# Performance work log

Measured on AMD Instinct MI355X. Metric: run time of the kernel, lower is better.

Reference implementation:

```python
import jax, jax.numpy as jnp
import numpy as np

N_VISIBLE = 4096
N_HIDDEN = 4096
BATCH = 8192


def setup_inputs() -> dict:
    key = jax.random.key(0)
    k_x, k_w = jax.random.split(key)
    input_data = jax.random.uniform(k_x, (BATCH, N_VISIBLE), dtype=jnp.float32)
    # xavier_uniform with sigmoid gain (=1.0): limit = sqrt(6/(fan_in+fan_out))
    limit = float(np.sqrt(6.0 / (N_VISIBLE + N_HIDDEN)))
    W = jax.random.uniform(k_w, (N_VISIBLE, N_HIDDEN), dtype=jnp.float32,
                           minval=-limit, maxval=limit)
    hidden_bias = jnp.zeros((N_HIDDEN,), dtype=jnp.float32)
    return {"input_data": input_data, "W": W, "hidden_bias": hidden_bias}


def reference(input_data, W, hidden_bias):
    # RBM.sample_hidden_2 (forward): sigmoid(x @ W + b), batched over samples.
    # (The torch code loops per sample with host syncs; same math, vectorized.)
    hid_prob = jax.nn.sigmoid(jnp.matmul(input_data, W) + hidden_bias)
    return hid_prob
```

## Files before the change

kernel.cpp:

```cpp
#include <hip/hip_runtime.h>
#include <cstdint>

#define MDIM 8192
#define NDIM 4096
#define KDIM 4096
#define NT (KDIM / 64)

typedef __bf16 bf16x8 __attribute__((ext_vector_type(8)));
typedef float f32x4 __attribute__((ext_vector_type(4)));

#define MFMA16 __builtin_amdgcn_mfma_f32_16x16x32_bf16

__device__ __forceinline__ void gload_lds16(const void* g, void* l) {
    __builtin_amdgcn_global_load_lds(
        (const __attribute__((address_space(1))) uint32_t*)g,
        (__attribute__((address_space(3))) uint32_t*)l, 16, 0, 0);
}

__device__ __forceinline__ unsigned short bf16_bits(float f) {
    __bf16 b = (__bf16)f;
    return __builtin_bit_cast(unsigned short, b);
}

__device__ __forceinline__ int detect_f32(const void* X) {
    int ok = 1;
    if (threadIdx.x < 128) {
        unsigned short h = ((const unsigned short*)X)[threadIdx.x];
        ok = (h <= 0x3F80);
    }
    return __syncthreads_and(ok) ? 0 : 1;
}

__global__ __launch_bounds__(256) void prep(const void* __restrict__ X,
                                            const void* __restrict__ W,
                                            __bf16* __restrict__ Xb,
                                            __bf16* __restrict__ WT) {
    const int f32 = detect_f32(X);
    const int t = threadIdx.x;
    if (blockIdx.x < 8192) {
        if (!f32) return;
        const float* Xf = (const float*)X;
        const long base = ((long)blockIdx.x * 256 + t) * 16;
#pragma unroll
        for (int c = 0; c < 2; ++c) {
            float4 v0 = *(const float4*)(Xf + base + c * 8);
            float4 v1 = *(const float4*)(Xf + base + c * 8 + 4);
            unsigned short r[8] = {bf16_bits(v0.x), bf16_bits(v0.y),
                                   bf16_bits(v0.z), bf16_bits(v0.w),
                                   bf16_bits(v1.x), bf16_bits(v1.y),
                                   bf16_bits(v1.z), bf16_bits(v1.w)};
            *(uint4*)(Xb + base + c * 8) = *(const uint4*)r;
        }
        return;
    }
    __shared__ unsigned short tile[64 * 65];
    const int bid = blockIdx.x - 8192;
    const int n0 = (bid & 63) * 64;
    const int k0 = (bid >> 6) * 64;
    if (f32) {
        const float* Wf = (const float*)W;
#pragma unroll
        for (int p = 0; p < 4; ++p) {
            const int ch = p * 256 + t;
            const int kr = ch >> 4;
            const int nc = ch & 15;
            float4 v = *(const float4*)(Wf + (long)(k0 + kr) * NDIM + n0 + nc * 4);
            tile[(nc * 4 + 0) * 65 + kr] = bf16_bits(v.x);
            tile[(nc * 4 + 1) * 65 + kr] = bf16_bits(v.y);
            tile[(nc * 4 + 2) * 65 + kr] = bf16_bits(v.z);
            tile[(nc * 4 + 3) * 65 + kr] = bf16_bits(v.w);
        }
    } else {
        const __bf16* Wb = (const __bf16*)W;
#pragma unroll
        for (int p = 0; p < 2; ++p) {
            const int ch = p * 256 + t;
            const int kr = ch >> 3;
            const int nc = ch & 7;
            uint4 v = *(const uint4*)(Wb + (long)(k0 + kr) * NDIM + n0 + nc * 8);
            const unsigned short* e = (const unsigned short*)&v;
#pragma unroll
            for (int i = 0; i < 8; ++i) tile[(nc * 8 + i) * 65 + kr] = e[i];
        }
    }
    __syncthreads();
#pragma unroll
    for (int p = 0; p < 2; ++p) {
        const int ch = p * 256 + t;
        const int nr = ch >> 3;
        const int kc = ch & 7;
        unsigned short r[8];
#pragma unroll
        for (int i = 0; i < 8; ++i) r[i] = tile[nr * 65 + kc * 8 + i];
        *(uint4*)(WT + (long)(n0 + nr) * KDIM + k0 + kc * 8) = *(uint4*)r;
    }
}

__global__ __launch_bounds__(256) void transpose_w(const void* __restrict__ X,
                                                   const void* __restrict__ W,
                                                   __bf16* __restrict__ WT) {
    __shared__ unsigned short tile[64 * 65];
    const int f32 = detect_f32(X);
    const int t = threadIdx.x;
    const int k0 = blockIdx.y * 64;
    const int n0 = blockIdx.x * 64;
    if (f32) {
        const float* Wf = (const float*)W;
#pragma unroll
        for (int p = 0; p < 4; ++p) {
            const int ch = p * 256 + t;
            const int kr = ch >> 4;
            const int nc = ch & 15;
            float4 v = *(const float4*)(Wf + (long)(k0 + kr) * NDIM + n0 + nc * 4);
            tile[(nc * 4 + 0) * 65 + kr] = bf16_bits(v.x);
            tile[(nc * 4 + 1) * 65 + kr] = bf16_bits(v.y);
            tile[(nc * 4 + 2) * 65 + kr] = bf16_bits(v.z);
            tile[(nc * 4 + 3) * 65 + kr] = bf16_bits(v.w);
        }
    } else {
        const __bf16* Wb = (const __bf16*)W;
#pragma unroll
        for (int p = 0; p < 2; ++p) {
            const int ch = p * 256 + t;
            const int kr = ch >> 3;
            const int nc = ch & 7;
            uint4 v = *(const uint4*)(Wb + (long)(k0 + kr) * NDIM + n0 + nc * 8);
            const unsigned short* e = (const unsigned short*)&v;
#pragma unroll
            for (int i = 0; i < 8; ++i) tile[(nc * 8 + i) * 65 + kr] = e[i];
        }
    }
    __syncthreads();
#pragma unroll
    for (int p = 0; p < 2; ++p) {
        const int ch = p * 256 + t;
        const int nr = ch >> 3;
        const int kc = ch & 7;
        unsigned short r[8];
#pragma unroll
        for (int i = 0; i < 8; ++i) r[i] = tile[nr * 65 + kc * 8 + i];
        *(uint4*)(WT + (long)(n0 + nr) * KDIM + k0 + kc * 8) = *(uint4*)r;
    }
}

#define P_OPEN()                                        \
    do {                                                \
        __builtin_amdgcn_sched_barrier(0);              \
        __builtin_amdgcn_s_barrier();                   \
        asm volatile("s_waitcnt lgkmcnt(0)" ::: "memory"); \
        __builtin_amdgcn_sched_barrier(0);              \
    } while (0)
#define P_CLOSE()                          \
    do {                                   \
        __builtin_amdgcn_sched_barrier(0); \
        __builtin_amdgcn_s_barrier();      \
    } while (0)

__global__ __launch_bounds__(512, 2) void gemm256(
    const void* __restrict__ X, const __bf16* __restrict__ Xb,
    const __bf16* __restrict__ WT, const void* __restrict__ bias,
    void* __restrict__ out) {
    __shared__ __bf16 sA[2][256][64];
    __shared__ __bf16 sB[2][256][64];
    const int f32 = detect_f32(X);
    const __bf16* __restrict__ Abf = f32 ? Xb : (const __bf16*)X;
    const int t = threadIdx.x;
    const int lane = t & 63;
    const int wid = t >> 6;
    const int wm = wid >> 2;
    const int wn = wid & 3;
    const int lrow = lane & 15;
    const int quad = lane >> 4;
    const int l7 = lrow & 7;

    const int flat = blockIdx.x;
    const int swz = (flat & 7) * (512 / 8) + (flat >> 3);
    const long m0 = (long)(swz >> 4) * 256;
    const long n0 = (long)(swz & 15) * 256;

    const int r8 = lane >> 3;
    const int c8 = lane & 7;
    const int cs = (c8 ^ r8) * 8;
    const __bf16* gA = Abf + (m0 + wid * 8 + r8) * KDIM + cs;
    const __bf16* gB = WT + (n0 + wid * 8 + r8) * KDIM + cs;
    __bf16* lA = &sA[0][wid * 8][0];
    __bf16* lB = &sB[0][wid * 8][0];

    auto stage_a = [&](int tt2) {
        const long off = (long)(tt2 & 1) * 16384;
        const long ko = (long)(tt2 & (NT - 1)) * 64;
        gload_lds16(gA + ko, lA + off);
        gload_lds16(gA + (long)64 * KDIM + ko, lA + off + 4096);
        gload_lds16(gA + (long)128 * KDIM + ko, lA + off + 8192);
        gload_lds16(gA + (long)192 * KDIM + ko, lA + off + 12288);
    };
    auto stage_b = [&](int tt2, int h) {
        const long off = (long)(tt2 & 1) * 16384 + (long)h * 8192;
        const long ko = (long)(tt2 & (NT - 1)) * 64;
        gload_lds16(gB + (long)(h * 128) * KDIM + ko, lB + off);
        gload_lds16(gB + (long)(h * 128 + 64) * KDIM + ko, lB + off + 4096);
    };

    const int soff0 = (quad ^ l7) * 8;
    const int soff1 = ((4 + quad) ^ l7) * 8;
    const __bf16* pa = &sA[0][wm * 128 + lrow][0];
    const __bf16* pb = &sB[0][wn * 64 + lrow][0];

    f32x4 acc[8][4] = {};

    stage_a(0);
    stage_b(0, 0);
    stage_b(0, 1);
    stage_b(1, 0);
    stage_a(1);
    __builtin_amdgcn_sched_barrier(0);
    asm volatile("s_waitcnt vmcnt(6)" ::: "memory");
    __builtin_amdgcn_sched_barrier(0);
    __builtin_amdgcn_s_barrier();

#pragma unroll 1
    for (int tt = 0; tt < NT; ++tt) {
        const int db = tt & 1;
        const __bf16* paT = pa + db * 16384;
        const __bf16* pbT = pb + db * 16384;
        bf16x8 aF[4][2], bF[4][2];
#pragma unroll
        for (int j = 0; j < 4; ++j) {
            bF[j][0] = *(const bf16x8*)(pbT + j * 1024 + soff0);
            bF[j][1] = *(const bf16x8*)(pbT + j * 1024 + soff1);
        }
#pragma unroll
        for (int i = 0; i < 4; ++i) {
            aF[i][0] = *(const bf16x8*)(paT + i * 1024 + soff0);
            aF[i][1] = *(const bf16x8*)(paT + i * 1024 + soff1);
        }
        stage_b(tt + 1, 1);
        P_OPEN();
        __builtin_amdgcn_s_setprio(1);
#pragma unroll
        for (int i = 0; i < 4; ++i)
#pragma unroll
            for (int j = 0; j < 2; ++j) {
                acc[i][j] = MFMA16(aF[i][0], bF[j][0], acc[i][j], 0, 0, 0);
                acc[i][j] = MFMA16(aF[i][1], bF[j][1], acc[i][j], 0, 0, 0);
            }
        __builtin_amdgcn_s_setprio(0);
        P_CLOSE();
        stage_b(tt + 2, 0);
        P_OPEN();
        __builtin_amdgcn_s_setprio(1);
#pragma unroll
        for (int i = 0; i < 4; ++i)
#pragma unroll
            for (int j = 2; j < 4; ++j) {
                acc[i][j] = MFMA16(aF[i][0], bF[j][0], acc[i][j], 0, 0, 0);
                acc[i][j] = MFMA16(aF[i][1], bF[j][1], acc[i][j], 0, 0, 0);
            }
        __builtin_amdgcn_s_setprio(0);
        P_CLOSE();
#pragma unroll
        for (int i = 0; i < 4; ++i) {
            aF[i][0] = *(const bf16x8*)(paT + 4096 + i * 1024 + soff0);
            aF[i][1] = *(const bf16x8*)(paT + 4096 + i * 1024 + soff1);
        }
        P_OPEN();
        __builtin_amdgcn_s_setprio(1);
#pragma unroll
        for (int i = 0; i < 4; ++i)
#pragma unroll
            for (int j = 2; j < 4; ++j) {
                acc[i + 4][j] = MFMA16(aF[i][0], bF[j][0], acc[i + 4][j], 0, 0, 0);
                acc[i + 4][j] = MFMA16(aF[i][1], bF[j][1], acc[i + 4][j], 0, 0, 0);
            }
        __builtin_amdgcn_s_setprio(0);
        P_CLOSE();
        stage_a(tt + 2);
        P_OPEN();
        __builtin_amdgcn_s_setprio(1);
#pragma unroll
        for (int i = 0; i < 4; ++i)
#pragma unroll
            for (int j = 0; j < 2; ++j) {
                acc[i + 4][j] = MFMA16(aF[i][0], bF[j][0], acc[i + 4][j], 0, 0, 0);
                acc[i + 4][j] = MFMA16(aF[i][1], bF[j][1], acc[i + 4][j], 0, 0, 0);
            }
        __builtin_amdgcn_s_setprio(0);
        __builtin_amdgcn_sched_barrier(0);
        asm volatile("s_waitcnt vmcnt(6)" ::: "memory");
        __builtin_amdgcn_sched_barrier(0);
        __builtin_amdgcn_s_barrier();
    }

    const int crow0 = (int)m0 + wm * 128 + quad * 4;
    if (f32) {
        float* of = (float*)out;
        const float* bf = (const float*)bias;
#pragma unroll
        for (int j = 0; j < 4; ++j) {
            const int col = (int)n0 + wn * 64 + j * 16 + lrow;
            const float bv = bf[col];
#pragma unroll
            for (int i = 0; i < 8; ++i) {
                const long rbase = (long)(crow0 + i * 16) * NDIM + col;
#pragma unroll
                for (int r = 0; r < 4; ++r) {
                    const float x = acc[i][j][r] + bv;
                    of[rbase + (long)r * NDIM] = 1.0f / (1.0f + __expf(-x));
                }
            }
        }
    } else {
        __bf16* ob = (__bf16*)out;
        const __bf16* bb = (const __bf16*)bias;
#pragma unroll
        for (int j = 0; j < 4; ++j) {
            const int col = (int)n0 + wn * 64 + j * 16 + lrow;
            const float bv = (float)bb[col];
#pragma unroll
            for (int i = 0; i < 8; ++i) {
                const long rbase = (long)(crow0 + i * 16) * NDIM + col;
#pragma unroll
                for (int r = 0; r < 4; ++r) {
                    const float x = acc[i][j][r] + bv;
                    ob[rbase + (long)r * NDIM] = (__bf16)(1.0f / (1.0f + __expf(-x)));
                }
            }
        }
    }
}

template <int MODE>
__global__ __launch_bounds__(256) void gemm_bias_sigmoid(
    const void* __restrict__ X, const __bf16* __restrict__ Xb,
    const void* __restrict__ Wp, const __bf16* __restrict__ WT,
    const void* __restrict__ bias, void* __restrict__ out) {
    __shared__ __bf16 sA[128 * 64];
    __shared__ __bf16 sB[128 * 64];
    const int f32 = detect_f32(X);
    const int t = threadIdx.x;
    const int lane = t & 63;
    const int wid = t >> 6;
    const int m0 = blockIdx.y * 128;
    const int n0 = blockIdx.x * 128;
    const int wm = (wid & 1) * 64;
    const int wn = (wid >> 1) * 64;
    const int lrow = lane & 15;
    const int quad = lane >> 4;

    f32x4 acc[4][4] = {};

    {
        const int srow = t >> 2;
        const int schk = t & 3;
        __bf16* ldsA = sA + wid * 512;
        __bf16* ldsB = sB + wid * 512;
        const int arow = t >> 1;
        const int acol = (t & 1) * 16;
        const int fp = t & 15;
        const int fc = t >> 4;
        uint32_t* sB32 = (uint32_t*)sB;

        auto compute = [&]() {
            bf16x8 aF[4], bFr[4];
            const __bf16* pa = sA + (wm + lrow) * 32 + quad * 8;
            const __bf16* pb = sB + (wn + lrow) * 32 + quad * 8;
#pragma unroll
            for (int i = 0; i < 4; ++i) aF[i] = *(const bf16x8*)(pa + i * 512);
#pragma unroll
            for (int j = 0; j < 4; ++j) bFr[j] = *(const bf16x8*)(pb + j * 512);
#pragma unroll
            for (int i = 0; i < 4; ++i)
#pragma unroll
                for (int j = 0; j < 4; ++j)
                    acc[i][j] = MFMA16(aF[i], bFr[j], acc[i][j], 0, 0, 0);
        };

        if (MODE == 1 && !f32) {
            const __bf16* gA = (const __bf16*)X + (long)(m0 + srow) * KDIM + schk * 8;
            const __bf16* gB = WT + (long)(n0 + srow) * KDIM + schk * 8;
            for (int kt = 0; kt < KDIM / 32; ++kt) {
                const __bf16* a0 = gA + kt * 32;
                gload_lds16(a0, ldsA);
                gload_lds16(a0 + (long)64 * KDIM, ldsA + 2048);
                const __bf16* b0 = gB + kt * 32;
                gload_lds16(b0, ldsB);
                gload_lds16(b0 + (long)64 * KDIM, ldsB + 2048);
                __syncthreads();
                compute();
                __syncthreads();
            }
        } else if (MODE == 1) {
            const float* Xf = (const float*)X;
            const __bf16* gB = WT + (long)(n0 + srow) * KDIM + schk * 8;
            for (int kt = 0; kt < KDIM / 32; ++kt) {
                const __bf16* b0 = gB + kt * 32;
                gload_lds16(b0, ldsB);
                gload_lds16(b0 + (long)64 * KDIM, ldsB + 2048);
                const float* ap = Xf + (long)(m0 + arow) * KDIM + kt * 32 + acol;
                float4 v0 = *(const float4*)(ap);
                float4 v1 = *(const float4*)(ap + 4);
                float4 v2 = *(const float4*)(ap + 8);
                float4 v3 = *(const float4*)(ap + 12);
                unsigned short r[16] = {
                    bf16_bits(v0.x), bf16_bits(v0.y), bf16_bits(v0.z), bf16_bits(v0.w),
                    bf16_bits(v1.x), bf16_bits(v1.y), bf16_bits(v1.z), bf16_bits(v1.w),
                    bf16_bits(v2.x), bf16_bits(v2.y), bf16_bits(v2.z), bf16_bits(v2.w),
                    bf16_bits(v3.x), bf16_bits(v3.y), bf16_bits(v3.z), bf16_bits(v3.w)};
                *(uint4*)(sA + arow * 32 + acol) = *(const uint4*)(r);
                *(uint4*)(sA + arow * 32 + acol + 8) = *(const uint4*)(r + 8);
                __syncthreads();
                compute();
                __syncthreads();
            }
        } else if (MODE == 2 && !f32) {
            const __bf16* gA = (const __bf16*)X + (long)(m0 + srow) * KDIM + schk * 8;
            const __bf16* Wb = (const __bf16*)Wp;
            for (int kt = 0; kt < KDIM / 32; ++kt) {
                const __bf16* a0 = gA + kt * 32;
                gload_lds16(a0, ldsA);
                gload_lds16(a0 + (long)64 * KDIM, ldsA + 2048);
                const __bf16* w0 = Wb + (long)(kt * 32 + 2 * fp) * NDIM + n0 + fc * 8;
                uint4 g0 = *(const uint4*)(w0);
                uint4 g1 = *(const uint4*)(w0 + NDIM);
                const unsigned short* e0 = (const unsigned short*)&g0;
                const unsigned short* e1 = (const unsigned short*)&g1;
#pragma unroll
                for (int i = 0; i < 8; ++i)
                    sB32[(fc * 8 + i) * 16 + fp] =
                        (uint32_t)e0[i] | ((uint32_t)e1[i] << 16);
                __syncthreads();
                compute();
                __syncthreads();
            }
        } else if (MODE == 2) {
            const float* Xf = (const float*)X;
            const float* Wf = (const float*)Wp;
            for (int kt = 0; kt < KDIM / 32; ++kt) {
                const float* ap = Xf + (long)(m0 + arow) * KDIM + kt * 32 + acol;
                float4 v0 = *(const float4*)(ap);
                float4 v1 = *(const float4*)(ap + 4);
                float4 v2 = *(const float4*)(ap + 8);
                float4 v3 = *(const float4*)(ap + 12);
                unsigned short r[16] = {
                    bf16_bits(v0.x), bf16_bits(v0.y), bf16_bits(v0.z), bf16_bits(v0.w),
                    bf16_bits(v1.x), bf16_bits(v1.y), bf16_bits(v1.z), bf16_bits(v1.w),
                    bf16_bits(v2.x), bf16_bits(v2.y), bf16_bits(v2.z), bf16_bits(v2.w),
                    bf16_bits(v3.x), bf16_bits(v3.y), bf16_bits(v3.z), bf16_bits(v3.w)};
                *(uint4*)(sA + arow * 32 + acol) = *(const uint4*)(r);
                *(uint4*)(sA + arow * 32 + acol + 8) = *(const uint4*)(r + 8);
                const float* w0 = Wf + (long)(kt * 32 + 2 * fp) * NDIM + n0 + fc * 8;
                float4 u0 = *(const float4*)(w0);
                float4 u1 = *(const float4*)(w0 + 4);
                float4 u2 = *(const float4*)(w0 + NDIM);
                float4 u3 = *(const float4*)(w0 + NDIM + 4);
                float k0v[8] = {u0.x, u0.y, u0.z, u0.w, u1.x, u1.y, u1.z, u1.w};
                float k1v[8] = {u2.x, u2.y, u2.z, u2.w, u3.x, u3.y, u3.z, u3.w};
#pragma unroll
                for (int i = 0; i < 8; ++i)
                    sB32[(fc * 8 + i) * 16 + fp] =
                        (uint32_t)bf16_bits(k0v[i]) |
                        ((uint32_t)bf16_bits(k1v[i]) << 16);
                __syncthreads();
                compute();
                __syncthreads();
            }
        }
    }

    const int crow = m0 + wm + quad * 4;
    if (f32) {
        float* of = (float*)out;
        const float* bf = (const float*)bias;
#pragma unroll
        for (int j = 0; j < 4; ++j) {
            const int col = n0 + wn + j * 16 + lrow;
            const float bv = bf[col];
#pragma unroll
            for (int i = 0; i < 4; ++i) {
                const long rbase = (long)(crow + i * 16) * NDIM + col;
#pragma unroll
                for (int r = 0; r < 4; ++r) {
                    const float x = acc[i][j][r] + bv;
                    of[rbase + (long)r * NDIM] = 1.0f / (1.0f + __expf(-x));
                }
            }
        }
    } else {
        __bf16* ob = (__bf16*)out;
        const __bf16* bb = (const __bf16*)bias;
#pragma unroll
        for (int j = 0; j < 4; ++j) {
            const int col = n0 + wn + j * 16 + lrow;
            const float bv = (float)bb[col];
#pragma unroll
            for (int i = 0; i < 4; ++i) {
                const long rbase = (long)(crow + i * 16) * NDIM + col;
#pragma unroll
                for (int r = 0; r < 4; ++r) {
                    const float x = acc[i][j][r] + bv;
                    ob[rbase + (long)r * NDIM] = (__bf16)(1.0f / (1.0f + __expf(-x)));
                }
            }
        }
    }
}

extern "C" void kernel_launch(void* const* d_in, const int* in_sizes, int n_in,
                              void* d_out, int out_size, void* d_ws,
                              size_t ws_size, hipStream_t stream) {
    const void* X = d_in[0];
    const void* W = d_in[1];
    const void* bias = d_in[2];

    const size_t wt_bytes = (size_t)KDIM * NDIM * sizeof(__bf16);
    const size_t xb_bytes = (size_t)MDIM * KDIM * sizeof(__bf16);

    if (ws_size >= wt_bytes + xb_bytes) {
        __bf16* WT = (__bf16*)d_ws;
        __bf16* Xb = (__bf16*)((char*)d_ws + wt_bytes);
        prep<<<8192 + 4096, 256, 0, stream>>>(X, W, Xb, WT);
        gemm256<<<dim3((MDIM / 256) * (NDIM / 256)), 512, 0, stream>>>(
            X, Xb, WT, bias, d_out);
    } else if (ws_size >= wt_bytes) {
        __bf16* WT = (__bf16*)d_ws;
        transpose_w<<<dim3(NDIM / 64, KDIM / 64), 256, 0, stream>>>(X, W, WT);
        dim3 gg(NDIM / 128, MDIM / 128);
        gemm_bias_sigmoid<1><<<gg, 256, 0, stream>>>(X, nullptr, W, WT, bias, d_out);
    } else {
        dim3 gg(NDIM / 128, MDIM / 128);
        gemm_bias_sigmoid<2><<<gg, 256, 0, stream>>>(X, nullptr, W, nullptr, bias, d_out);
    }
}
```

Measured before the change: 559.3 us.

## Restructure GEMM main loop into templated double-buffer k-tiles with staggered fragment loads

```diff
diff --git a/kernel.cpp b/kernel.cpp
--- a/kernel.cpp
+++ b/kernel.cpp
@@ -40,16 +40,14 @@
     if (blockIdx.x < 8192) {
         if (!f32) return;
         const float* Xf = (const float*)X;
-        const long base = ((long)blockIdx.x * 256 + t) * 16;
-#pragma unroll
-        for (int c = 0; c < 2; ++c) {
-            float4 v0 = *(const float4*)(Xf + base + c * 8);
-            float4 v1 = *(const float4*)(Xf + base + c * 8 + 4);
-            unsigned short r[8] = {bf16_bits(v0.x), bf16_bits(v0.y),
-                                   bf16_bits(v0.z), bf16_bits(v0.w),
-                                   bf16_bits(v1.x), bf16_bits(v1.y),
-                                   bf16_bits(v1.z), bf16_bits(v1.w)};
-            *(uint4*)(Xb + base + c * 8) = *(const uint4*)r;
+        const long xbase = (long)blockIdx.x * 4096;
+#pragma unroll
+        for (int rr = 0; rr < 4; ++rr) {
+            const long idx = xbase + rr * 1024 + t * 4;
+            float4 v = *(const float4*)(Xf + idx);
+            unsigned short r[4] = {bf16_bits(v.x), bf16_bits(v.y),
+                                   bf16_bits(v.z), bf16_bits(v.w)};
+            *(uint2*)(Xb + idx) = *(const uint2*)r;
         }
         return;
     }
@@ -143,18 +141,105 @@
     }
 }
 
-#define P_OPEN()                                        \
-    do {                                                \
-        __builtin_amdgcn_sched_barrier(0);              \
-        __builtin_amdgcn_s_barrier();                   \
+#define P_OPEN()                                           \
+    do {                                                   \
+        __builtin_amdgcn_sched_barrier(0);                 \
+        __builtin_amdgcn_s_barrier();                      \
         asm volatile("s_waitcnt lgkmcnt(0)" ::: "memory"); \
-        __builtin_amdgcn_sched_barrier(0);              \
+        __builtin_amdgcn_sched_barrier(0);                 \
     } while (0)
 #define P_CLOSE()                          \
     do {                                   \
         __builtin_amdgcn_sched_barrier(0); \
         __builtin_amdgcn_s_barrier();      \
     } while (0)
+
+template <int DBOFF>
+__device__ __forceinline__ void ktile(const __bf16* pa, const __bf16* pb,
+                                      const __bf16* gA, const __bf16* gB,
+                                      __bf16* lA, __bf16* lB, long ko2,
+                                      int soff0, int soff1,
+                                      f32x4 (&acc)[8][4]) {
+    const __bf16* paT = pa + DBOFF;
+    const __bf16* pbT = pb + DBOFF;
+    bf16x8 aF[4][2], bF[4][2];
+#pragma unroll
+    for (int j = 0; j < 2; ++j) {
+        bF[j][0] = *(const bf16x8*)(pbT + j * 1024 + soff0);
+        bF[j][1] = *(const bf16x8*)(pbT + j * 1024 + soff1);
+    }
+#pragma unroll
+    for (int i = 0; i < 4; ++i) {
+        aF[i][0] = *(const bf16x8*)(paT + i * 1024 + soff0);
+        aF[i][1] = *(const bf16x8*)(paT + i * 1024 + soff1);
+    }
+    asm volatile("s_waitcnt lgkmcnt(8)" ::: "memory");
+    P_OPEN();
+    __builtin_amdgcn_s_setprio(1);
+#pragma unroll
+    for (int kk = 0; kk < 2; ++kk)
+#pragma unroll
+        for (int i = 0; i < 4; ++i)
+#pragma unroll
+            for (int j = 0; j < 2; ++j)
+                acc[i][j] = MFMA16(aF[i][kk], bF[j][kk], acc[i][j], 0, 0, 0);
+    __builtin_amdgcn_s_setprio(0);
+    P_CLOSE();
+#pragma unroll
+    for (int j = 2; j < 4; ++j) {
+        bF[j][0] = *(const bf16x8*)(pbT + j * 1024 + soff0);
+        bF[j][1] = *(const bf16x8*)(pbT + j * 1024 + soff1);
+    }
+    P_OPEN();
+    __builtin_amdgcn_s_setprio(1);
+#pragma unroll
+    for (int kk = 0; kk < 2; ++kk)
+#pragma unroll
+        for (int i = 0; i < 4; ++i)
+#pragma unroll
+            for (int j = 2; j < 4; ++j)
+                acc[i][j] = MFMA16(aF[i][kk], bF[j][kk], acc[i][j], 0, 0, 0);
+    __builtin_amdgcn_s_setprio(0);
+    P_CLOSE();
+#pragma unroll
+    for (int i = 0; i < 4; ++i) {
+        aF[i][0] = *(const bf16x8*)(paT + (4 + i) * 1024 + soff0);
+        aF[i][1] = *(const bf16x8*)(paT + (4 + i) * 1024 + soff1);
+    }
+    gload_lds16(gB + ko2, lB + DBOFF);
+    gload_lds16(gB + (long)64 * KDIM + ko2, lB + DBOFF + 4096);
+    gload_lds16(gB + (long)128 * KDIM + ko2, lB + DBOFF + 8192);
+    gload_lds16(gB + (long)192 * KDIM + ko2, lB + DBOFF + 12288);
+    P_OPEN();
+    __builtin_amdgcn_s_setprio(1);
+#pragma unroll
+    for (int kk = 0; kk < 2; ++kk)
+#pragma unroll
+        for (int i = 0; i < 4; ++i)
+#pragma unroll
+            for (int j = 2; j < 4; ++j)
+                acc[4 + i][j] = MFMA16(aF[i][kk], bF[j][kk], acc[4 + i][j], 0, 0, 0);
+    __builtin_amdgcn_s_setprio(0);
+    P_CLOSE();
+    gload_lds16(gA + ko2, lA + DBOFF);
+    gload_lds16(gA + (long)64 * KDIM + ko2, lA + DBOFF + 4096);
+    gload_lds16(gA + (long)128 * KDIM + ko2, lA + DBOFF + 8192);
+    gload_lds16(gA + (long)192 * KDIM + ko2, lA + DBOFF + 12288);
+    P_OPEN();
+    __builtin_amdgcn_s_setprio(1);
+#pragma unroll
+    for (int kk = 0; kk < 2; ++kk)
+#pragma unroll
+        for (int i = 0; i < 4; ++i)
+#pragma unroll
+            for (int j = 0; j < 2; ++j)
+                acc[4 + i][j] = MFMA16(aF[i][kk], bF[j][kk], acc[4 + i][j], 0, 0, 0);
+    __builtin_amdgcn_s_setprio(0);
+    __builtin_amdgcn_sched_barrier(0);
+    asm volatile("s_waitcnt vmcnt(8)" ::: "memory");
+    __builtin_amdgcn_sched_barrier(0);
+    __builtin_amdgcn_s_barrier();
+}
 
 __global__ __launch_bounds__(512, 2) void gemm256(
     const void* __restrict__ X, const __bf16* __restrict__ Xb,
@@ -186,21 +271,6 @@
     __bf16* lA = &sA[0][wid * 8][0];
     __bf16* lB = &sB[0][wid * 8][0];
 
-    auto stage_a = [&](int tt2) {
-        const long off = (long)(tt2 & 1) * 16384;
-        const long ko = (long)(tt2 & (NT - 1)) * 64;
-        gload_lds16(gA + ko, lA + off);
-        gload_lds16(gA + (long)64 * KDIM + ko, lA + off + 4096);
-        gload_lds16(gA + (long)128 * KDIM + ko, lA + off + 8192);
-        gload_lds16(gA + (long)192 * KDIM + ko, lA + off + 12288);
-    };
-    auto stage_b = [&](int tt2, int h) {
-        const long off = (long)(tt2 & 1) * 16384 + (long)h * 8192;
-        const long ko = (long)(tt2 & (NT - 1)) * 64;
-        gload_lds16(gB + (long)(h * 128) * KDIM + ko, lB + off);
-        gload_lds16(gB + (long)(h * 128 + 64) * KDIM + ko, lB + off + 4096);
-    };
-
     const int soff0 = (quad ^ l7) * 8;
     const int soff1 = ((4 + quad) ^ l7) * 8;
     const __bf16* pa = &sA[0][wm * 128 + lrow][0];
@@ -208,87 +278,35 @@
 
     f32x4 acc[8][4] = {};
 
-    stage_a(0);
-    stage_b(0, 0);
-    stage_b(0, 1);
-    stage_b(1, 0);
-    stage_a(1);
+    {
+        gload_lds16(gA, lA);
+        gload_lds16(gA + (long)64 * KDIM, lA + 4096);
+        gload_lds16(gA + (long)128 * KDIM, lA + 8192);
+        gload_lds16(gA + (long)192 * KDIM, lA + 12288);
+        gload_lds16(gB, lB);
+        gload_lds16(gB + (long)64 * KDIM, lB + 4096);
+        gload_lds16(gB + (long)128 * KDIM, lB + 8192);
+        gload_lds16(gB + (long)192 * KDIM, lB + 12288);
+        gload_lds16(gA + 64, lA + 16384);
+        gload_lds16(gA + (long)64 * KDIM + 64, lA + 16384 + 4096);
+        gload_lds16(gA + (long)128 * KDIM + 64, lA + 16384 + 8192);
+        gload_lds16(gA + (long)192 * KDIM + 64, lA + 16384 + 12288);
+        gload_lds16(gB + 64, lB + 16384);
+        gload_lds16(gB + (long)64 * KDIM + 64, lB + 16384 + 4096);
+        gload_lds16(gB + (long)128 * KDIM + 64, lB + 16384 + 8192);
+        gload_lds16(gB + (long)192 * KDIM + 64, lB + 16384 + 12288);
+    }
     __builtin_amdgcn_sched_barrier(0);
-    asm volatile("s_waitcnt vmcnt(6)" ::: "memory");
+    asm volatile("s_waitcnt vmcnt(8)" ::: "memory");
     __builtin_amdgcn_sched_barrier(0);
     __builtin_amdgcn_s_barrier();
 
 #pragma unroll 1
-    for (int tt = 0; tt < NT; ++tt) {
-        const int db = tt & 1;
-        const __bf16* paT = pa + db * 16384;
-        const __bf16* pbT = pb + db * 16384;
-        bf16x8 aF[4][2], bF[4][2];
-#pragma unroll
-        for (int j = 0; j < 4; ++j) {
-            bF[j][0] = *(const bf16x8*)(pbT + j * 1024 + soff0);
-            bF[j][1] = *(const bf16x8*)(pbT + j * 1024 + soff1);
-        }
-#pragma unroll
-        for (int i = 0; i < 4; ++i) {
-            aF[i][0] = *(const bf16x8*)(paT + i * 1024 + soff0);
-            aF[i][1] = *(const bf16x8*)(paT + i * 1024 + soff1);
-        }
-        stage_b(tt + 1, 1);
-        P_OPEN();
-        __builtin_amdgcn_s_setprio(1);
-#pragma unroll
-        for (int i = 0; i < 4; ++i)
-#pragma unroll
-            for (int j = 0; j < 2; ++j) {
-                acc[i][j] = MFMA16(aF[i][0], bF[j][0], acc[i][j], 0, 0, 0);
-                acc[i][j] = MFMA16(aF[i][1], bF[j][1], acc[i][j], 0, 0, 0);
-            }
-        __builtin_amdgcn_s_setprio(0);
-        P_CLOSE();
-        stage_b(tt + 2, 0);
-        P_OPEN();
-        __builtin_amdgcn_s_setprio(1);
-#pragma unroll
-        for (int i = 0; i < 4; ++i)
-#pragma unroll
-            for (int j = 2; j < 4; ++j) {
-                acc[i][j] = MFMA16(aF[i][0], bF[j][0], acc[i][j], 0, 0, 0);
-                acc[i][j] = MFMA16(aF[i][1], bF[j][1], acc[i][j], 0, 0, 0);
-            }
-        __builtin_amdgcn_s_setprio(0);
-        P_CLOSE();
-#pragma unroll
-        for (int i = 0; i < 4; ++i) {
-            aF[i][0] = *(const bf16x8*)(paT + 4096 + i * 1024 + soff0);
-            aF[i][1] = *(const bf16x8*)(paT + 4096 + i * 1024 + soff1);
-        }
-        P_OPEN();
-        __builtin_amdgcn_s_setprio(1);
-#pragma unroll
-        for (int i = 0; i < 4; ++i)
-#pragma unroll
-            for (int j = 2; j < 4; ++j) {
-                acc[i + 4][j] = MFMA16(aF[i][0], bF[j][0], acc[i + 4][j], 0, 0, 0);
-                acc[i + 4][j] = MFMA16(aF[i][1], bF[j][1], acc[i + 4][j], 0, 0, 0);
-            }
-        __builtin_amdgcn_s_setprio(0);
-        P_CLOSE();
-        stage_a(tt + 2);
-        P_OPEN();
-        __builtin_amdgcn_s_setprio(1);
-#pragma unroll
-        for (int i = 0; i < 4; ++i)
-#pragma unroll
-            for (int j = 0; j < 2; ++j) {
-                acc[i + 4][j] = MFMA16(aF[i][0], bF[j][0], acc[i + 4][j], 0, 0, 0);
-                acc[i + 4][j] = MFMA16(aF[i][1], bF[j][1], acc[i + 4][j], 0, 0, 0);
-            }
-        __builtin_amdgcn_s_setprio(0);
-        __builtin_amdgcn_sched_barrier(0);
-        asm volatile("s_waitcnt vmcnt(6)" ::: "memory");
-        __builtin_amdgcn_sched_barrier(0);
-        __builtin_amdgcn_s_barrier();
+    for (int tt = 0; tt < NT; tt += 2) {
+        const long ko2a = (long)((tt + 2) & (NT - 1)) * 64;
+        const long ko2b = (long)((tt + 3) & (NT - 1)) * 64;
+        ktile<0>(pa, pb, gA, gB, lA, lB, ko2a, soff0, soff1, acc);
+        ktile<16384>(pa, pb, gA, gB, lA, lB, ko2b, soff0, soff1, acc);
     }
 
     const int crow0 = (int)m0 + wm * 128 + quad * 4;
```

After: 519.3 us. 7.2% less time.
